# Optimization experiments

Measured on AMD Instinct MI355X. Metric: run time of the kernel, lower is better.

Reference implementation:

```python
import jax, jax.numpy as jnp
import numpy as np

DIM = 512
WIN = 8
HEADS = 16
HEAD_DIM = DIM // HEADS
N = WIN * WIN
B_ = 1568


def _rel_pos_idx(window_size: int) -> np.ndarray:
    ch = np.arange(window_size)
    cw = np.arange(window_size)
    coords = np.stack(np.meshgrid(ch, cw, indexing='ij'))  # [2, W, W]
    flat = coords.reshape(2, -1)                            # [2, N]
    rel = flat[:, :, None] - flat[:, None, :]               # [2, N, N]
    rel = rel.transpose(1, 2, 0).copy()                     # [N, N, 2]
    rel[:, :, 0] += window_size - 1
    rel[:, :, 1] += window_size - 1
    rel[:, :, 0] *= 2 * window_size - 1
    return rel.sum(-1).astype(np.int32)                     # [N, N]


def setup_inputs() -> dict:
    key = jax.random.key(0)
    kx, kt, kq, kp, kb = jax.random.split(key, 5)
    x = jax.random.normal(kx, (B_, N, DIM), dtype=jnp.float32)
    # learned params
    table = jax.random.normal(kt, ((2 * WIN - 1) ** 2, HEADS), dtype=jnp.float32) * 0.02
    qkv_w = jax.random.normal(kq, (3 * DIM, DIM), dtype=jnp.float32) * (1.0 / np.sqrt(DIM))
    proj_w = jax.random.normal(kp, (DIM, DIM), dtype=jnp.float32) * (1.0 / np.sqrt(DIM))
    proj_b = jax.random.normal(kb, (DIM,), dtype=jnp.float32) * 0.02
    rel_idx = jnp.asarray(_rel_pos_idx(WIN))  # [N, N] int32
    return {"x": x, "qkv_w": qkv_w, "table": table, "proj_w": proj_w,
            "proj_b": proj_b, "rel_idx": rel_idx}


def reference(x, qkv_w, table, proj_w, proj_b, rel_idx):
    Bw, n, c = x.shape
    scale = jnp.sqrt(jnp.float32(HEAD_DIM))
    # qkv: Linear no-bias, torch weight [3C, C] -> x @ W^T
    qkv = (x @ qkv_w.T).reshape(Bw, n, 3, HEADS, HEAD_DIM)
    qkv = jnp.transpose(qkv, (2, 0, 3, 1, 4))  # [3, B, H, N, hd]
    q, k, v = qkv[0], qkv[1], qkv[2]
    attn = jnp.einsum('bhnd,bhmd->bhnm', q, k) / scale  # [B, H, N, N]
    bias = table[rel_idx]                                # [N, N, H]
    attn = attn + jnp.transpose(bias, (2, 0, 1))[None]   # [B, H, N, N]
    attn = jax.nn.softmax(attn, axis=-1)
    out = jnp.einsum('bhnm,bhmd->bhnd', attn, v)         # [B, H, N, hd]
    out = jnp.transpose(out, (0, 2, 1, 3)).reshape(Bw, n, c)
    return out @ proj_w.T + proj_b
```

## Files before the change

kernel.cpp:

```cpp
#include <hip/hip_runtime.h>
#include <stdint.h>

typedef unsigned short ushort_t;
typedef __attribute__((ext_vector_type(4))) float f32x4;
typedef __attribute__((ext_vector_type(8))) short s16x8;

#define S1_ELEMS ((size_t)1568*64*512)

__device__ __forceinline__ ushort_t f2bf(float f) {
  unsigned u = __builtin_bit_cast(unsigned, f);
  u = u + 0x7fffu + ((u >> 16) & 1u);
  return (ushort_t)(u >> 16);
}

__device__ __forceinline__ void gl_lds16(const ushort_t* g, ushort_t* l) {
  typedef __attribute__((address_space(1))) void gvoid;
  typedef __attribute__((address_space(3))) void lvoid;
  __builtin_amdgcn_global_load_lds((gvoid*)(ushort_t*)g, (lvoid*)l, 16, 0, 0);
}

__global__ void k_convert_hi(const float* __restrict__ src, ushort_t* __restrict__ hi, long n4) {
  long i = (long)blockIdx.x * blockDim.x + threadIdx.x;
  long stride = (long)gridDim.x * blockDim.x;
  for (; i < n4; i += stride) {
    float4 v = ((const float4*)src)[i];
    ushort4 h;
    h.x = f2bf(v.x); h.y = f2bf(v.y); h.z = f2bf(v.z); h.w = f2bf(v.w);
    ((ushort4*)hi)[i] = h;
  }
}

__global__ void k_bias(const float* __restrict__ table, const int* __restrict__ rel_idx,
                       float* __restrict__ bias) {
  int i = blockIdx.x * 256 + threadIdx.x;
  int h = i >> 12, rc = i & 4095;
  bias[i] = table[rel_idx[rc] * 16 + h];
}

struct GemmCtx {
  ushort_t* lds;
  const ushort_t *pA0, *pA1, *pB0, *pB1;
  int w, lane, wm, wn;
};

template<int BUFP, int KH, int RH, int SSEL, int SBUFP, int SU, int VM>
__device__ __forceinline__ void phase(const GemmCtx& C, f32x4 (&acc)[8][4], s16x8 (&bf)[4], int stau) {
  s16x8 af[4];
  #pragma unroll
  for (int t = 0; t < 4; t++)
    af[t] = *(const s16x8*)&C.lds[BUFP*32768 + ((C.wm*8 + RH*4 + t)*2 + KH)*512 + C.lane*8];
  if constexpr (RH == 0) {
    #pragma unroll
    for (int t = 0; t < 4; t++)
      bf[t] = *(const s16x8*)&C.lds[BUFP*32768 + 16384 + ((C.wn*4 + t)*2 + KH)*512 + C.lane*8];
  }
  if constexpr (SSEL == 0) {
    gl_lds16(C.pA0 + stau*64 + SU*32, C.lds + SBUFP*32768 + (4*C.w + SU)*512);
    gl_lds16(C.pA1 + stau*64 + SU*32, C.lds + SBUFP*32768 + (4*C.w + 2 + SU)*512);
  } else if constexpr (SSEL == 1) {
    gl_lds16(C.pB0 + stau*64 + SU*32, C.lds + SBUFP*32768 + 16384 + (4*C.w + SU)*512);
    gl_lds16(C.pB1 + stau*64 + SU*32, C.lds + SBUFP*32768 + 16384 + (4*C.w + 2 + SU)*512);
  }
  if constexpr (VM == 8) asm volatile("s_waitcnt vmcnt(8)" ::: "memory");
  else if constexpr (VM == 4) asm volatile("s_waitcnt vmcnt(4)" ::: "memory");
  else if constexpr (VM == 0) asm volatile("s_waitcnt vmcnt(0)" ::: "memory");
  __builtin_amdgcn_s_barrier();
  __builtin_amdgcn_s_setprio(1);
  #pragma unroll
  for (int ta = 0; ta < 4; ta++)
    #pragma unroll
    for (int tb = 0; tb < 4; tb++)
      acc[RH*4 + ta][tb] = __builtin_amdgcn_mfma_f32_16x16x32_bf16(af[ta], bf[tb], acc[RH*4 + ta][tb], 0, 0, 0);
  __builtin_amdgcn_s_setprio(0);
  __builtin_amdgcn_s_barrier();
}

template<int BUFP, bool S12, bool S34, int VM2, int VM4>
__device__ __forceinline__ void ktile(const GemmCtx& C, f32x4 (&acc)[8][4], int tau) {
  s16x8 bf[4];
  phase<BUFP, 0, 0, S12 ? 0 : -1, BUFP^1, 1, -1 >(C, acc, bf, tau + 1);
  phase<BUFP, 0, 1, S12 ? 1 : -1, BUFP^1, 1, VM2>(C, acc, bf, tau + 1);
  phase<BUFP, 1, 0, S34 ? 0 : -1, BUFP,   0, -1 >(C, acc, bf, tau + 2);
  phase<BUFP, 1, 1, S34 ? 1 : -1, BUFP,   0, VM4>(C, acc, bf, tau + 2);
}

__global__ __launch_bounds__(512, 2) void k_gemm_qkv(
    const ushort_t* __restrict__ xh, const ushort_t* __restrict__ wh,
    ushort_t* __restrict__ qh, ushort_t* __restrict__ kh, ushort_t* __restrict__ vt) {
  extern __shared__ __align__(16) ushort_t lds[];
  const int tid = threadIdx.x, w = tid >> 6, lane = tid & 63;
  const int g = lane >> 4, l15 = lane & 15;
  const int wm = w >> 2, wn = w & 3;
  int flat = blockIdx.x;
  int swz = (flat & 7) * 294 + (flat >> 3);
  int bx = swz % 6, by = swz / 6;

  GemmCtx C;
  C.lds = lds;
  C.pA0 = xh + ((size_t)by*256 + (size_t)(2*w)*16 + l15)*512 + g*8;
  C.pA1 = C.pA0 + 16*512;
  C.pB0 = wh + ((size_t)bx*256 + (size_t)(2*w)*16 + l15)*512 + g*8;
  C.pB1 = C.pB0 + 16*512;
  C.w = w; C.lane = lane; C.wm = wm; C.wn = wn;

  f32x4 acc[8][4];
  #pragma unroll
  for (int r = 0; r < 8; r++)
    #pragma unroll
    for (int c = 0; c < 4; c++) acc[r][c] = (f32x4){0.f, 0.f, 0.f, 0.f};

  gl_lds16(C.pA0 +  0, lds + (4*w + 0)*512);
  gl_lds16(C.pA1 +  0, lds + (4*w + 2)*512);
  gl_lds16(C.pB0 +  0, lds + 16384 + (4*w + 0)*512);
  gl_lds16(C.pB1 +  0, lds + 16384 + (4*w + 2)*512);
  gl_lds16(C.pA0 + 32, lds + (4*w + 1)*512);
  gl_lds16(C.pA1 + 32, lds + (4*w + 3)*512);
  gl_lds16(C.pB0 + 32, lds + 16384 + (4*w + 1)*512);
  gl_lds16(C.pB1 + 32, lds + 16384 + (4*w + 3)*512);
  gl_lds16(C.pA0 + 64, lds + 32768 + (4*w + 0)*512);
  gl_lds16(C.pA1 + 64, lds + 32768 + (4*w + 2)*512);
  gl_lds16(C.pB0 + 64, lds + 32768 + 16384 + (4*w + 0)*512);
  gl_lds16(C.pB1 + 64, lds + 32768 + 16384 + (4*w + 2)*512);
  asm volatile("s_waitcnt vmcnt(4)" ::: "memory");
  __builtin_amdgcn_s_barrier();

  for (int kt = 0; kt < 6; kt += 2) {
    ktile<0, true, true, 8, 8>(C, acc, kt);
    ktile<1, true, true, 8, 8>(C, acc, kt + 1);
  }
  ktile<0, true,  false, 8, 4>(C, acc, 6);
  ktile<1, false, false, 0, -1>(C, acc, 7);

  asm volatile("" ::: "memory");

  const int sel = bx >> 1;
  #pragma unroll
  for (int ra = 0; ra < 8; ra++)
    #pragma unroll
    for (int tb = 0; tb < 4; tb++)
      #pragma unroll
      for (int j = 0; j < 4; j++) {
        int row = wm*128 + ra*16 + g*4 + j;
        int col = wn*64 + tb*16 + l15;
        int b_i = row >> 6, n = row & 63, h_i = col >> 5, d = col & 31;
        int addr = (sel == 2) ? ((b_i*8 + h_i)*2048 + d*64 + n)
                              : ((b_i*8 + h_i)*2048 + n*32 + d);
        lds[addr] = f2bf(acc[ra][tb][j]);
      }
  asm volatile("s_waitcnt lgkmcnt(0)" ::: "memory");
  __builtin_amdgcn_s_barrier();
  ushort_t* dst = (sel == 0) ? qh : (sel == 1) ? kh : vt;
  const int hbase = (bx & 1) * 8;
  #pragma unroll
  for (int it = 0; it < 16; it++) {
    int cg = it*512 + tid;
    int region = cg >> 8, inner = cg & 255;
    int b_i = region >> 3, h_i = region & 7;
    s16x8 v = *(const s16x8*)&lds[region*2048 + inner*8];
    int b = by*4 + b_i, h = hbase + h_i;
    *(s16x8*)&dst[(size_t)(b*16 + h)*2048 + inner*8] = v;
  }
}

__global__ __launch_bounds__(256) void k_attn(
    const ushort_t* __restrict__ qh, const ushort_t* __restrict__ kh,
    const ushort_t* __restrict__ vt, const float* __restrict__ bias,
    ushort_t* __restrict__ aoh) {
  __shared__ ushort_t plds[4][64*72];
  const int tid = threadIdx.x, w = tid >> 6, lane = tid & 63;
  const int g = lane >> 4, l15 = lane & 15;
  const int gw = blockIdx.x * 4 + w;
  const int b = gw >> 4, h = gw & 15;
  const size_t base = (size_t)(b*16 + h) * 2048;

  s16x8 qf[4], kf[4];
  #pragma unroll
  for (int t = 0; t < 4; t++) {
    size_t o = base + (size_t)(t*16 + l15)*32 + g*8;
    qf[t] = *(const s16x8*)&qh[o];
    kf[t] = *(const s16x8*)&kh[o];
  }
  s16x8 vf[2][2];
  #pragma unroll
  for (int kt = 0; kt < 2; kt++)
    #pragma unroll
    for (int nt = 0; nt < 2; nt++)
      vf[kt][nt] = *(const s16x8*)&vt[base + (size_t)(nt*16 + l15)*64 + kt*32 + g*8];

  f32x4 s[4][4];
  #pragma unroll
  for (int r = 0; r < 4; r++)
    #pragma unroll
    for (int c = 0; c < 4; c++) s[r][c] = (f32x4){0.f,0.f,0.f,0.f};
  #pragma unroll
  for (int r = 0; r < 4; r++)
    #pragma unroll
    for (int c = 0; c < 4; c++)
      s[r][c] = __builtin_amdgcn_mfma_f32_16x16x32_bf16(qf[r], kf[c], s[r][c], 0, 0, 0);

  const float invs = 0.17677669529663687f;
  const float* bh_ = bias + ((size_t)h << 12);
  #pragma unroll
  for (int r = 0; r < 4; r++)
    #pragma unroll
    for (int c = 0; c < 4; c++)
      #pragma unroll
      for (int j = 0; j < 4; j++) {
        int rr = r*16 + g*4 + j, cc = c*16 + l15;
        s[r][c][j] = s[r][c][j]*invs + bh_[rr*64 + cc];
      }

  #pragma unroll
  for (int r = 0; r < 4; r++)
    #pragma unroll
    for (int j = 0; j < 4; j++) {
      float mx = fmaxf(fmaxf(s[r][0][j], s[r][1][j]), fmaxf(s[r][2][j], s[r][3][j]));
      mx = fmaxf(mx, __shfl_xor(mx, 1));
      mx = fmaxf(mx, __shfl_xor(mx, 2));
      mx = fmaxf(mx, __shfl_xor(mx, 4));
      mx = fmaxf(mx, __shfl_xor(mx, 8));
      float p0 = __expf(s[r][0][j]-mx), p1 = __expf(s[r][1][j]-mx);
      float p2 = __expf(s[r][2][j]-mx), p3 = __expf(s[r][3][j]-mx);
      float sum = p0 + p1 + p2 + p3;
      sum += __shfl_xor(sum, 1);
      sum += __shfl_xor(sum, 2);
      sum += __shfl_xor(sum, 4);
      sum += __shfl_xor(sum, 8);
      float rv = 1.0f / sum;
      s[r][0][j] = p0*rv; s[r][1][j] = p1*rv; s[r][2][j] = p2*rv; s[r][3][j] = p3*rv;
    }

  ushort_t* Pm = plds[w];
  #pragma unroll
  for (int r = 0; r < 4; r++)
    #pragma unroll
    for (int c = 0; c < 4; c++)
      #pragma unroll
      for (int j = 0; j < 4; j++) {
        int rr = r*16 + g*4 + j, cc = c*16 + l15;
        Pm[rr*72 + cc] = f2bf(s[r][c][j]);
      }
  s16x8 pf[4][2];
  #pragma unroll
  for (int ta = 0; ta < 4; ta++)
    #pragma unroll
    for (int kt = 0; kt < 2; kt++)
      pf[ta][kt] = *(const s16x8*)&Pm[(ta*16 + l15)*72 + kt*32 + g*8];

  f32x4 o[4][2];
  #pragma unroll
  for (int ta = 0; ta < 4; ta++)
    #pragma unroll
    for (int nt = 0; nt < 2; nt++) o[ta][nt] = (f32x4){0.f,0.f,0.f,0.f};
  #pragma unroll
  for (int ta = 0; ta < 4; ta++)
    #pragma unroll
    for (int nt = 0; nt < 2; nt++)
      #pragma unroll
      for (int kt = 0; kt < 2; kt++)
        o[ta][nt] = __builtin_amdgcn_mfma_f32_16x16x32_bf16(pf[ta][kt], vf[kt][nt], o[ta][nt], 0, 0, 0);

  #pragma unroll
  for (int ta = 0; ta < 4; ta++)
    #pragma unroll
    for (int nt = 0; nt < 2; nt++)
      #pragma unroll
      for (int j = 0; j < 4; j++) {
        int rr = ta*16 + g*4 + j, dd = nt*16 + l15;
        aoh[((size_t)b*64 + rr)*512 + h*32 + dd] = f2bf(o[ta][nt][j]);
      }
}

__global__ __launch_bounds__(256) void k_gemm_proj(
    const ushort_t* __restrict__ ah, const ushort_t* __restrict__ wh,
    const float* __restrict__ pb, float* __restrict__ out) {
  __shared__ __align__(16) ushort_t lds0[16896];
  const int tid = threadIdx.x, w = tid >> 6, lane = tid & 63;
  const int g = lane >> 4, l15 = lane & 15;
  int flat = blockIdx.x;
  int swz = (flat & 7) * 392 + (flat >> 3);
  int bx = swz & 3, by = swz >> 2;
  const int wm = w >> 1, wn = w & 1;

  f32x4 acc[4][4];
  #pragma unroll
  for (int r = 0; r < 4; r++)
    #pragma unroll
    for (int c = 0; c < 4; c++) acc[r][c] = (f32x4){0.f,0.f,0.f,0.f};

  const ushort_t* sptr[8]; int loff[8];
  #pragma unroll
  for (int q = 0; q < 8; q++) {
    int gq = w*8 + q;
    int buf = gq >> 4, ti = gq & 15, s = ti >> 1, u = ti & 1;
    const ushort_t* src = buf ? wh : ah;
    size_t rb = buf ? (size_t)bx*128 : (size_t)by*128;
    sptr[q] = src + (rb + (size_t)(s*16 + l15))*512 + u*32 + g*8;
    loff[q] = buf*8192 + ti*512;
  }

  for (int kk = 0; kk < 512; kk += 64) {
    #pragma unroll
    for (int q = 0; q < 8; q++) gl_lds16(sptr[q] + kk, lds0 + loff[q]);
    __syncthreads();
    #pragma unroll
    for (int u = 0; u < 2; u++) {
      s16x8 af[4], bf[4];
      #pragma unroll
      for (int t = 0; t < 4; t++) {
        af[t] = *(const s16x8*)&lds0[((wm*4 + t)*2 + u)*512 + lane*8];
        bf[t] = *(const s16x8*)&lds0[8192 + ((wn*4 + t)*2 + u)*512 + lane*8];
      }
      #pragma unroll
      for (int r = 0; r < 4; r++)
        #pragma unroll
        for (int c = 0; c < 4; c++)
          acc[r][c] = __builtin_amdgcn_mfma_f32_16x16x32_bf16(af[r], bf[c], acc[r][c], 0, 0, 0);
    }
    __syncthreads();
  }

  float* Tf = (float*)lds0;
  const int PF = 132;
  #pragma unroll
  for (int half = 0; half < 2; half++) {
    if (wm == half) {
      #pragma unroll
      for (int r = 0; r < 4; r++)
        #pragma unroll
        for (int c = 0; c < 4; c++)
          #pragma unroll
          for (int j = 0; j < 4; j++)
            Tf[(r*16 + g*4 + j)*PF + wn*64 + c*16 + l15] = acc[r][c][j];
    }
    __syncthreads();
    #pragma unroll
    for (int p = 0; p < 8; p++) {
      int ch = p*256 + tid;
      int row = ch >> 5, c4 = ch & 31;
      f32x4 v = *(const f32x4*)&Tf[row*PF + c4*4];
      int ncol = bx*128 + c4*4;
      f32x4 pbv = *(const f32x4*)&pb[ncol];
      v = v + pbv;
      *(f32x4*)&out[(size_t)(by*128 + half*64 + row)*512 + ncol] = v;
    }
    __syncthreads();
  }
}

extern "C" void kernel_launch(void* const* d_in, const int* in_sizes, int n_in,
                              void* d_out, int out_size, void* d_ws, size_t ws_size,
                              hipStream_t stream) {
  const float* x      = (const float*)d_in[0];
  const float* qkv_w  = (const float*)d_in[1];
  const float* table  = (const float*)d_in[2];
  const float* proj_w = (const float*)d_in[3];
  const float* proj_b = (const float*)d_in[4];
  const int*   rel_idx = (const int*)d_in[5];

  const size_t S1 = S1_ELEMS;
  const size_t need = (4*S1 + 786432 + 262144)*sizeof(ushort_t) + 65536*sizeof(float);
  if (ws_size < need) return;

  ushort_t* qh  = (ushort_t*)d_ws;
  ushort_t* kh  = qh + S1;
  ushort_t* vt  = kh + S1;
  ushort_t* xh  = vt + S1;
  ushort_t* wqh = xh + S1;
  ushort_t* wph = wqh + 786432;
  float*    bias = (float*)(wph + 262144);
  ushort_t* aoh = xh;

  hipFuncSetAttribute((const void*)k_gemm_qkv,
                      hipFuncAttributeMaxDynamicSharedMemorySize, 131072);

  k_convert_hi<<<2048, 256, 0, stream>>>(x, xh, (long)(S1/4));
  k_convert_hi<<<768, 256, 0, stream>>>(qkv_w, wqh, 196608);
  k_convert_hi<<<256, 256, 0, stream>>>(proj_w, wph, 65536);
  k_bias<<<256, 256, 0, stream>>>(table, rel_idx, bias);
  k_gemm_qkv<<<2352, 512, 131072, stream>>>(xh, wqh, qh, kh, vt);
  k_attn<<<6272, 256, 0, stream>>>(qh, kh, vt, bias, aoh);
  k_gemm_proj<<<3136, 256, 0, stream>>>(aoh, wph, proj_b, (float*)d_out);
}
```

Measured before the change: 591.9 us.

## Share 256x256 double-buffered GEMM loop between QKV and projection kernels

Replaces the phase-templated QKV main loop with a simpler shared double-buffered 256x256 loop that prefetches the next K tile while issuing MFMAs in two halves. Rewrites the projection GEMM to use the same 512-thread 256x256 tile (784 blocks instead of 3136 small ones), with a swizzled fp32 LDS epilogue. It also XOR-swizzles the QKV epilogue LDS layout and packs V-transpose stores into 64-bit writes to cut bank conflicts. The simpler loop waits on vmcnt(0) every iteration, so it may lose some of the finer-grained overlap of the old schedule.

```diff
diff --git a/kernel.cpp b/kernel.cpp
--- a/kernel.cpp
+++ b/kernel.cpp
@@ -2,6 +2,7 @@
 #include <stdint.h>
 
 typedef unsigned short ushort_t;
+typedef unsigned long long u64_t;
 typedef __attribute__((ext_vector_type(4))) float f32x4;
 typedef __attribute__((ext_vector_type(8))) short s16x8;
 
@@ -37,51 +38,72 @@
   bias[i] = table[rel_idx[rc] * 16 + h];
 }
 
-struct GemmCtx {
-  ushort_t* lds;
-  const ushort_t *pA0, *pA1, *pB0, *pB1;
-  int w, lane, wm, wn;
-};
-
-template<int BUFP, int KH, int RH, int SSEL, int SBUFP, int SU, int VM>
-__device__ __forceinline__ void phase(const GemmCtx& C, f32x4 (&acc)[8][4], s16x8 (&bf)[4], int stau) {
-  s16x8 af[4];
-  #pragma unroll
-  for (int t = 0; t < 4; t++)
-    af[t] = *(const s16x8*)&C.lds[BUFP*32768 + ((C.wm*8 + RH*4 + t)*2 + KH)*512 + C.lane*8];
-  if constexpr (RH == 0) {
+__device__ __forceinline__ void gemm256_loop(
+    ushort_t* lds, const ushort_t* pA, const ushort_t* pB,
+    int w, int lane, int wm, int wn, f32x4 (&acc)[8][4]) {
+  #pragma unroll
+  for (int q = 0; q < 2; q++) {
+    gl_lds16(pA + q*8192 +  0, lds + ((2*w + q)*2 + 0)*512);
+    gl_lds16(pA + q*8192 + 32, lds + ((2*w + q)*2 + 1)*512);
+    gl_lds16(pB + q*8192 +  0, lds + 16384 + ((2*w + q)*2 + 0)*512);
+    gl_lds16(pB + q*8192 + 32, lds + 16384 + ((2*w + q)*2 + 1)*512);
+  }
+  asm volatile("s_waitcnt vmcnt(0)" ::: "memory");
+  __builtin_amdgcn_s_barrier();
+
+  for (int tau = 0; tau < 8; ++tau) {
+    ushort_t* bufR = lds + (tau & 1)*32768;
+    ushort_t* bufW = lds + ((tau & 1) ^ 1)*32768;
+    if (tau < 7) {
+      int ko = (tau + 1)*64;
+      #pragma unroll
+      for (int q = 0; q < 2; q++) {
+        gl_lds16(pA + q*8192 + ko,      bufW + ((2*w + q)*2 + 0)*512);
+        gl_lds16(pA + q*8192 + ko + 32, bufW + ((2*w + q)*2 + 1)*512);
+        gl_lds16(pB + q*8192 + ko,      bufW + 16384 + ((2*w + q)*2 + 0)*512);
+        gl_lds16(pB + q*8192 + ko + 32, bufW + 16384 + ((2*w + q)*2 + 1)*512);
+      }
+    }
+    s16x8 af[4][2], bf[4][2];
     #pragma unroll
     for (int t = 0; t < 4; t++)
-      bf[t] = *(const s16x8*)&C.lds[BUFP*32768 + 16384 + ((C.wn*4 + t)*2 + KH)*512 + C.lane*8];
-  }
-  if constexpr (SSEL == 0) {
-    gl_lds16(C.pA0 + stau*64 + SU*32, C.lds + SBUFP*32768 + (4*C.w + SU)*512);
-    gl_lds16(C.pA1 + stau*64 + SU*32, C.lds + SBUFP*32768 + (4*C.w + 2 + SU)*512);
-  } else if constexpr (SSEL == 1) {
-    gl_lds16(C.pB0 + stau*64 + SU*32, C.lds + SBUFP*32768 + 16384 + (4*C.w + SU)*512);
-    gl_lds16(C.pB1 + stau*64 + SU*32, C.lds + SBUFP*32768 + 16384 + (4*C.w + 2 + SU)*512);
-  }
-  if constexpr (VM == 8) asm volatile("s_waitcnt vmcnt(8)" ::: "memory");
-  else if constexpr (VM == 4) asm volatile("s_waitcnt vmcnt(4)" ::: "memory");
-  else if constexpr (VM == 0) asm volatile("s_waitcnt vmcnt(0)" ::: "memory");
-  __builtin_amdgcn_s_barrier();
-  __builtin_amdgcn_s_setprio(1);
-  #pragma unroll
-  for (int ta = 0; ta < 4; ta++)
-    #pragma unroll
-    for (int tb = 0; tb < 4; tb++)
-      acc[RH*4 + ta][tb] = __builtin_amdgcn_mfma_f32_16x16x32_bf16(af[ta], bf[tb], acc[RH*4 + ta][tb], 0, 0, 0);
-  __builtin_amdgcn_s_setprio(0);
-  __builtin_amdgcn_s_barrier();
-}
-
-template<int BUFP, bool S12, bool S34, int VM2, int VM4>
-__device__ __forceinline__ void ktile(const GemmCtx& C, f32x4 (&acc)[8][4], int tau) {
-  s16x8 bf[4];
-  phase<BUFP, 0, 0, S12 ? 0 : -1, BUFP^1, 1, -1 >(C, acc, bf, tau + 1);
-  phase<BUFP, 0, 1, S12 ? 1 : -1, BUFP^1, 1, VM2>(C, acc, bf, tau + 1);
-  phase<BUFP, 1, 0, S34 ? 0 : -1, BUFP,   0, -1 >(C, acc, bf, tau + 2);
-  phase<BUFP, 1, 1, S34 ? 1 : -1, BUFP,   0, VM4>(C, acc, bf, tau + 2);
+      #pragma unroll
+      for (int kh = 0; kh < 2; kh++) {
+        af[t][kh] = *(const s16x8*)&bufR[((wm*8 + t)*2 + kh)*512 + lane*8];
+        bf[t][kh] = *(const s16x8*)&bufR[16384 + ((wn*4 + t)*2 + kh)*512 + lane*8];
+      }
+    __builtin_amdgcn_s_barrier();
+    asm volatile("s_waitcnt lgkmcnt(0)" ::: "memory");
+    __builtin_amdgcn_sched_barrier(0);
+    __builtin_amdgcn_s_setprio(1);
+    #pragma unroll
+    for (int t = 0; t < 4; t++)
+      #pragma unroll
+      for (int tb = 0; tb < 4; tb++) {
+        acc[t][tb] = __builtin_amdgcn_mfma_f32_16x16x32_bf16(af[t][0], bf[tb][0], acc[t][tb], 0, 0, 0);
+        acc[t][tb] = __builtin_amdgcn_mfma_f32_16x16x32_bf16(af[t][1], bf[tb][1], acc[t][tb], 0, 0, 0);
+      }
+    __builtin_amdgcn_s_setprio(0);
+    s16x8 ag[4][2];
+    #pragma unroll
+    for (int t = 0; t < 4; t++)
+      #pragma unroll
+      for (int kh = 0; kh < 2; kh++)
+        ag[t][kh] = *(const s16x8*)&bufR[((wm*8 + 4 + t)*2 + kh)*512 + lane*8];
+    asm volatile("s_waitcnt lgkmcnt(0)" ::: "memory");
+    __builtin_amdgcn_sched_barrier(0);
+    __builtin_amdgcn_s_setprio(1);
+    #pragma unroll
+    for (int t = 0; t < 4; t++)
+      #pragma unroll
+      for (int tb = 0; tb < 4; tb++) {
+        acc[4 + t][tb] = __builtin_amdgcn_mfma_f32_16x16x32_bf16(ag[t][0], bf[tb][0], acc[4 + t][tb], 0, 0, 0);
+        acc[4 + t][tb] = __builtin_amdgcn_mfma_f32_16x16x32_bf16(ag[t][1], bf[tb][1], acc[4 + t][tb], 0, 0, 0);
+      }
+    __builtin_amdgcn_s_setprio(0);
+    asm volatile("s_waitcnt vmcnt(0)" ::: "memory");
+    __builtin_amdgcn_s_barrier();
+  }
 }
 
 __global__ __launch_bounds__(512, 2) void k_gemm_qkv(
@@ -95,13 +117,8 @@
   int swz = (flat & 7) * 294 + (flat >> 3);
   int bx = swz % 6, by = swz / 6;
 
-  GemmCtx C;
-  C.lds = lds;
-  C.pA0 = xh + ((size_t)by*256 + (size_t)(2*w)*16 + l15)*512 + g*8;
-  C.pA1 = C.pA0 + 16*512;
-  C.pB0 = wh + ((size_t)bx*256 + (size_t)(2*w)*16 + l15)*512 + g*8;
-  C.pB1 = C.pB0 + 16*512;
-  C.w = w; C.lane = lane; C.wm = wm; C.wn = wn;
+  const ushort_t* pA = xh + ((size_t)by*256 + (size_t)(2*w)*16 + l15)*512 + g*8;
+  const ushort_t* pB = wh + ((size_t)bx*256 + (size_t)(2*w)*16 + l15)*512 + g*8;
 
   f32x4 acc[8][4];
   #pragma unroll
@@ -109,44 +126,41 @@
     #pragma unroll
     for (int c = 0; c < 4; c++) acc[r][c] = (f32x4){0.f, 0.f, 0.f, 0.f};
 
-  gl_lds16(C.pA0 +  0, lds + (4*w + 0)*512);
-  gl_lds16(C.pA1 +  0, lds + (4*w + 2)*512);
-  gl_lds16(C.pB0 +  0, lds + 16384 + (4*w + 0)*512);
-  gl_lds16(C.pB1 +  0, lds + 16384 + (4*w + 2)*512);
-  gl_lds16(C.pA0 + 32, lds + (4*w + 1)*512);
-  gl_lds16(C.pA1 + 32, lds + (4*w + 3)*512);
-  gl_lds16(C.pB0 + 32, lds + 16384 + (4*w + 1)*512);
-  gl_lds16(C.pB1 + 32, lds + 16384 + (4*w + 3)*512);
-  gl_lds16(C.pA0 + 64, lds + 32768 + (4*w + 0)*512);
-  gl_lds16(C.pA1 + 64, lds + 32768 + (4*w + 2)*512);
-  gl_lds16(C.pB0 + 64, lds + 32768 + 16384 + (4*w + 0)*512);
-  gl_lds16(C.pB1 + 64, lds + 32768 + 16384 + (4*w + 2)*512);
-  asm volatile("s_waitcnt vmcnt(4)" ::: "memory");
-  __builtin_amdgcn_s_barrier();
-
-  for (int kt = 0; kt < 6; kt += 2) {
-    ktile<0, true, true, 8, 8>(C, acc, kt);
-    ktile<1, true, true, 8, 8>(C, acc, kt + 1);
-  }
-  ktile<0, true,  false, 8, 4>(C, acc, 6);
-  ktile<1, false, false, 0, -1>(C, acc, 7);
+  gemm256_loop(lds, pA, pB, w, lane, wm, wn, acc);
 
   asm volatile("" ::: "memory");
-
   const int sel = bx >> 1;
-  #pragma unroll
-  for (int ra = 0; ra < 8; ra++)
-    #pragma unroll
-    for (int tb = 0; tb < 4; tb++)
-      #pragma unroll
-      for (int j = 0; j < 4; j++) {
-        int row = wm*128 + ra*16 + g*4 + j;
+  if (sel < 2) {
+    #pragma unroll
+    for (int ra = 0; ra < 8; ra++)
+      #pragma unroll
+      for (int tb = 0; tb < 4; tb++)
+        #pragma unroll
+        for (int j = 0; j < 4; j++) {
+          int row = wm*128 + ra*16 + g*4 + j;
+          int col = wn*64 + tb*16 + l15;
+          int r = (row >> 6)*8 + (col >> 5);
+          int n = row & 63, d = col & 31;
+          int byte = r*4096 + ((n*64 + d*2) ^ ((n & 12) << 3));
+          *(ushort_t*)((char*)lds + byte) = f2bf(acc[ra][tb][j]);
+        }
+  } else {
+    #pragma unroll
+    for (int ra = 0; ra < 8; ra++)
+      #pragma unroll
+      for (int tb = 0; tb < 4; tb++) {
+        int row0 = wm*128 + ra*16 + g*4;
         int col = wn*64 + tb*16 + l15;
-        int b_i = row >> 6, n = row & 63, h_i = col >> 5, d = col & 31;
-        int addr = (sel == 2) ? ((b_i*8 + h_i)*2048 + d*64 + n)
-                              : ((b_i*8 + h_i)*2048 + n*32 + d);
-        lds[addr] = f2bf(acc[ra][tb][j]);
-      }
+        int r = (row0 >> 6)*8 + (col >> 5);
+        int n0 = row0 & 63, d = col & 31;
+        u64_t pk = (u64_t)f2bf(acc[ra][tb][0])
+                 | ((u64_t)f2bf(acc[ra][tb][1]) << 16)
+                 | ((u64_t)f2bf(acc[ra][tb][2]) << 32)
+                 | ((u64_t)f2bf(acc[ra][tb][3]) << 48);
+        int byte = r*4096 + ((d*128 + n0*2) ^ ((d & 7) << 4) ^ (((((d >> 3) ^ (n0 >> 3))) & 1) << 6));
+        *(u64_t*)((char*)lds + byte) = pk;
+      }
+  }
   asm volatile("s_waitcnt lgkmcnt(0)" ::: "memory");
   __builtin_amdgcn_s_barrier();
   ushort_t* dst = (sel == 0) ? qh : (sel == 1) ? kh : vt;
@@ -154,11 +168,68 @@
   #pragma unroll
   for (int it = 0; it < 16; it++) {
     int cg = it*512 + tid;
-    int region = cg >> 8, inner = cg & 255;
-    int b_i = region >> 3, h_i = region & 7;
-    s16x8 v = *(const s16x8*)&lds[region*2048 + inner*8];
-    int b = by*4 + b_i, h = hbase + h_i;
+    int r = cg >> 8, inner = cg & 255;
+    int byte;
+    if (sel < 2) byte = r*4096 + ((inner*16) ^ (((inner >> 2) & 12) << 3));
+    else         byte = r*4096 + ((inner*16) ^ (((inner >> 3) & 7) << 4) ^ ((((inner >> 6) ^ inner) & 1) << 6));
+    s16x8 v = *(const s16x8*)((const char*)lds + byte);
+    int b = by*4 + (r >> 3), h = hbase + (r & 7);
     *(s16x8*)&dst[(size_t)(b*16 + h)*2048 + inner*8] = v;
+  }
+}
+
+__global__ __launch_bounds__(512, 2) void k_gemm_proj(
+    const ushort_t* __restrict__ ah, const ushort_t* __restrict__ wh,
+    const float* __restrict__ pb, float* __restrict__ out) {
+  extern __shared__ __align__(16) ushort_t lds[];
+  const int tid = threadIdx.x, w = tid >> 6, lane = tid & 63;
+  const int g = lane >> 4, l15 = lane & 15;
+  const int wm = w >> 2, wn = w & 3;
+  int flat = blockIdx.x;
+  int swz = (flat & 7) * 98 + (flat >> 3);
+  int bx = swz & 1, by = swz >> 1;
+
+  const ushort_t* pA = ah + ((size_t)by*256 + (size_t)(2*w)*16 + l15)*512 + g*8;
+  const ushort_t* pB = wh + ((size_t)bx*256 + (size_t)(2*w)*16 + l15)*512 + g*8;
+
+  f32x4 acc[8][4];
+  #pragma unroll
+  for (int r = 0; r < 8; r++)
+    #pragma unroll
+    for (int c = 0; c < 4; c++) acc[r][c] = (f32x4){0.f, 0.f, 0.f, 0.f};
+
+  gemm256_loop(lds, pA, pB, w, lane, wm, wn, acc);
+
+  asm volatile("" ::: "memory");
+  #pragma unroll
+  for (int p = 0; p < 2; p++) {
+    if (p) { asm volatile("" ::: "memory"); __builtin_amdgcn_s_barrier(); }
+    if (wm == p) {
+      #pragma unroll
+      for (int ra = 0; ra < 8; ra++)
+        #pragma unroll
+        for (int tb = 0; tb < 4; tb++)
+          #pragma unroll
+          for (int j = 0; j < 4; j++) {
+            int row = ra*16 + g*4 + j;
+            int col = wn*64 + tb*16 + l15;
+            int byte = (row*1024 + col*4) ^ ((row & 12) << 2) ^ ((row & 8) << 3);
+            *(float*)((char*)lds + byte) = acc[ra][tb][j];
+          }
+    }
+    asm volatile("s_waitcnt lgkmcnt(0)" ::: "memory");
+    __builtin_amdgcn_s_barrier();
+    #pragma unroll
+    for (int it = 0; it < 16; it++) {
+      int cg = it*512 + tid;
+      int row = cg >> 6, c16 = cg & 63;
+      int byte = row*1024 + ((c16*16) ^ ((row & 12) << 2) ^ ((row & 8) << 3));
+      f32x4 v = *(const f32x4*)((const char*)lds + byte);
+      int ncol = bx*256 + c16*4;
+      f32x4 pbv = *(const f32x4*)&pb[ncol];
+      v = v + pbv;
+      *(f32x4*)&out[(size_t)(by*256 + p*128 + row)*512 + ncol] = v;
+    }
   }
 }
 
@@ -271,83 +342,6 @@
       }
 }
 
-__global__ __launch_bounds__(256) void k_gemm_proj(
-    const ushort_t* __restrict__ ah, const ushort_t* __restrict__ wh,
-    const float* __restrict__ pb, float* __restrict__ out) {
-  __shared__ __align__(16) ushort_t lds0[16896];
-  const int tid = threadIdx.x, w = tid >> 6, lane = tid & 63;
-  const int g = lane >> 4, l15 = lane & 15;
-  int flat = blockIdx.x;
-  int swz = (flat & 7) * 392 + (flat >> 3);
-  int bx = swz & 3, by = swz >> 2;
-  const int wm = w >> 1, wn = w & 1;
-
-  f32x4 acc[4][4];
-  #pragma unroll
-  for (int r = 0; r < 4; r++)
-    #pragma unroll
-    for (int c = 0; c < 4; c++) acc[r][c] = (f32x4){0.f,0.f,0.f,0.f};
-
-  const ushort_t* sptr[8]; int loff[8];
-  #pragma unroll
-  for (int q = 0; q < 8; q++) {
-    int gq = w*8 + q;
-    int buf = gq >> 4, ti = gq & 15, s = ti >> 1, u = ti & 1;
-    const ushort_t* src = buf ? wh : ah;
-    size_t rb = buf ? (size_t)bx*128 : (size_t)by*128;
-    sptr[q] = src + (rb + (size_t)(s*16 + l15))*512 + u*32 + g*8;
-    loff[q] = buf*8192 + ti*512;
-  }
-
-  for (int kk = 0; kk < 512; kk += 64) {
-    #pragma unroll
-    for (int q = 0; q < 8; q++) gl_lds16(sptr[q] + kk, lds0 + loff[q]);
-    __syncthreads();
-    #pragma unroll
-    for (int u = 0; u < 2; u++) {
-      s16x8 af[4], bf[4];
-      #pragma unroll
-      for (int t = 0; t < 4; t++) {
-        af[t] = *(const s16x8*)&lds0[((wm*4 + t)*2 + u)*512 + lane*8];
-        bf[t] = *(const s16x8*)&lds0[8192 + ((wn*4 + t)*2 + u)*512 + lane*8];
-      }
-      #pragma unroll
-      for (int r = 0; r < 4; r++)
-        #pragma unroll
-        for (int c = 0; c < 4; c++)
-          acc[r][c] = __builtin_amdgcn_mfma_f32_16x16x32_bf16(af[r], bf[c], acc[r][c], 0, 0, 0);
-    }
-    __syncthreads();
-  }
-
-  float* Tf = (float*)lds0;
-  const int PF = 132;
-  #pragma unroll
-  for (int half = 0; half < 2; half++) {
-    if (wm == half) {
-      #pragma unroll
-      for (int r = 0; r < 4; r++)
-        #pragma unroll
-        for (int c = 0; c < 4; c++)
-          #pragma unroll
-          for (int j = 0; j < 4; j++)
-            Tf[(r*16 + g*4 + j)*PF + wn*64 + c*16 + l15] = acc[r][c][j];
-    }
-    __syncthreads();
-    #pragma unroll
-    for (int p = 0; p < 8; p++) {
-      int ch = p*256 + tid;
-      int row = ch >> 5, c4 = ch & 31;
-      f32x4 v = *(const f32x4*)&Tf[row*PF + c4*4];
-      int ncol = bx*128 + c4*4;
-      f32x4 pbv = *(const f32x4*)&pb[ncol];
-      v = v + pbv;
-      *(f32x4*)&out[(size_t)(by*128 + half*64 + row)*512 + ncol] = v;
-    }
-    __syncthreads();
-  }
-}
-
 extern "C" void kernel_launch(void* const* d_in, const int* in_sizes, int n_in,
                               void* d_out, int out_size, void* d_ws, size_t ws_size,
                               hipStream_t stream) {
@@ -373,6 +367,8 @@
 
   hipFuncSetAttribute((const void*)k_gemm_qkv,
                       hipFuncAttributeMaxDynamicSharedMemorySize, 131072);
+  hipFuncSetAttribute((const void*)k_gemm_proj,
+                      hipFuncAttributeMaxDynamicSharedMemorySize, 131072);
 
   k_convert_hi<<<2048, 256, 0, stream>>>(x, xh, (long)(S1/4));
   k_convert_hi<<<768, 256, 0, stream>>>(qkv_w, wqh, 196608);
@@ -380,5 +376,5 @@
   k_bias<<<256, 256, 0, stream>>>(table, rel_idx, bias);
   k_gemm_qkv<<<2352, 512, 131072, stream>>>(xh, wqh, qh, kh, vt);
   k_attn<<<6272, 256, 0, stream>>>(qh, kh, vt, bias, aoh);
-  k_gemm_proj<<<3136, 256, 0, stream>>>(aoh, wph, proj_b, (float*)d_out);
-}
+  k_gemm_proj<<<784, 512, 131072, stream>>>(aoh, wph, proj_b, (float*)d_out);
+}
```

After: 558.2 us. 1.06x faster.
